# Optimization experiments

Hardware: AMD Instinct MI355X
Metric: run time of the kernel (lower is better)

## Reference

```python
import jax, jax.numpy as jnp
import numpy as np

H = 16          # num_heads
WIN = 512       # window_size


def setup_inputs() -> dict:
    key = jax.random.key(0)
    ks = jax.random.split(key, 4)
    B, S, D = 1, 4096, 1024
    s = 1.0 / np.sqrt(D)
    x = jax.random.normal(ks[0], (B, S, D), jnp.float32)
    Wqkv = jax.random.normal(ks[1], (3 * D, D), jnp.float32) * s
    bqkv = jnp.zeros((3 * D,), jnp.float32)
    Wout = jax.random.normal(ks[2], (D, D), jnp.float32) * s
    bout = jnp.zeros((D,), jnp.float32)
    return {"x": x, "Wqkv": Wqkv, "bqkv": bqkv, "Wout": Wout, "bout": bout}


def reference(x, Wqkv, bqkv, Wout, bout):
    B, S, D = x.shape
    d = D // H
    pads = WIN // 2
    C = WIN                 # chunk of query tokens processed together
    N = S // C              # number of chunks
    L = C + WIN - 1         # key-block length covering all windows in a chunk

    qkv = (x @ Wqkv.T + bqkv).reshape(B, S, 3, H, d).transpose(2, 0, 3, 1, 4)
    q, k, v = qkv[0], qkv[1], qkv[2]          # [B,H,S,d]

    # zero-pad K/V exactly like F.pad(..., value=0.0) in the original
    kp = jnp.pad(k, ((0, 0), (0, 0), (pads, pads), (0, 0)))
    vp = jnp.pad(v, ((0, 0), (0, 0), (pads, pads), (0, 0)))

    # gather overlapping key/value blocks: chunk n covers padded idx [n*C, n*C+L)
    idx = jnp.arange(N)[:, None] * C + jnp.arange(L)[None, :]   # [N,L]
    kb = kp[:, :, idx, :]                      # [B,H,N,L,d]
    vb = vp[:, :, idx, :]
    qc = q.reshape(B, H, N, C, d)

    scores = jnp.einsum('bhncd,bhnld->bhncl', qc, kb) / np.sqrt(d).astype(np.float32)
    c = jnp.arange(C)[:, None]
    j = jnp.arange(L)[None, :]
    band = (j >= c) & (j < c + WIN)            # [C,L]; zero-pad keys stay IN (score 0), matching original
    scores = jnp.where(band, scores, -jnp.inf)
    attn = jax.nn.softmax(scores, axis=-1)

    o = jnp.einsum('bhncl,bhnld->bhncd', attn, vb).reshape(B, H, S, d)
    o = o.transpose(0, 2, 1, 3).reshape(B, S, D)
    return o @ Wout.T + bout
```

## Files before the change

kernel.cpp:

```cpp
#include <hip/hip_runtime.h>


typedef __bf16 bf16x8 __attribute__((ext_vector_type(8)));
typedef float f32x4 __attribute__((ext_vector_type(4)));
typedef unsigned short u16;
typedef unsigned int u32;

#define MFMA16(a, b, c) __builtin_amdgcn_mfma_f32_16x16x32_bf16(a, b, c, 0, 0, 0)

__device__ __forceinline__ u16 f2b(float f) {
  union { float f; u32 u; } x; x.f = f;
  u32 r = x.u + 0x7fffu + ((x.u >> 16) & 1u);
  return (u16)(r >> 16);
}

union U8x16 { int4 v; u16 u[8]; };

__device__ __forceinline__ void gll16(const u16* g, u16* l) {
  __builtin_amdgcn_global_load_lds(
      (const __attribute__((address_space(1))) u16*)g,
      (__attribute__((address_space(3))) u16*)l, 16, 0, 0);
}

__global__ void cvt_all(const float* __restrict__ x, const float* __restrict__ wqkv,
                        const float* __restrict__ wout, u16* __restrict__ dst,
                        u16* __restrict__ Kp, u16* __restrict__ VTp)
{
  const int i = blockIdx.x * blockDim.x + threadIdx.x;
  if (i < 1048576) {
    const float* src; int off;
    if (i < 524288)       { src = x;    off = i; }
    else if (i < 917504)  { src = wqkv; off = i - 524288; }
    else                  { src = wout; off = i - 917504; }
    const float4 a = ((const float4*)src)[off * 2];
    const float4 b = ((const float4*)src)[off * 2 + 1];
    U8x16 t;
    t.u[0] = f2b(a.x); t.u[1] = f2b(a.y); t.u[2] = f2b(a.z); t.u[3] = f2b(a.w);
    t.u[4] = f2b(b.x); t.u[5] = f2b(b.y); t.u[6] = f2b(b.z); t.u[7] = f2b(b.w);
    ((int4*)dst)[i] = t.v;
    return;
  }
  const int j = i - 1048576;
  const int4 z = {0, 0, 0, 0};
  if (j < 65536) {
    const int h = j >> 12, rem = j & 4095;
    const int row512 = rem >> 3, c8 = (rem & 7) * 8;
    const int row = (row512 < 256) ? row512 : (4096 + row512);
    *(int4*)(&Kp[((long)h * 4608 + row) * 64 + c8]) = z;
  } else {
    const int j2 = j - 65536;
    const int h = j2 >> 12, rem = j2 & 4095;
    const int d = rem >> 6, kc = rem & 63;
    const int key = (kc < 32) ? kc * 8 : (4096 + kc * 8);
    *(int4*)(&VTp[((long)h * 64 + d) * 4608 + key]) = z;
  }
}

__global__ __launch_bounds__(256, 6) void gemm_qkv(
    const u16* __restrict__ A, const u16* __restrict__ B,
    const float* __restrict__ bias,
    u16* __restrict__ Qb, u16* __restrict__ Kp, u16* __restrict__ VTp)
{
  __shared__ u16 smem[12288];
  u16* const As = smem;
  u16* const Bs = smem + 4096;

  const int K = 1024;
  const int tid  = threadIdx.x;
  const int lane = tid & 63;
  const int wave = tid >> 6;
  const int quad = lane >> 4;
  const int c16  = lane & 15;
  const int wr   = wave >> 1;
  const int wc   = wave & 1;
  const long m0 = (long)blockIdx.y * 64;
  const long n0 = (long)blockIdx.x * 128;

  const int rowo   = lane >> 3;
  const int schunk = (lane & 7) ^ rowo;
  const u16* gA0 = &A[(m0 + wave * 16 + rowo) * K + schunk * 8];
  const u16* gA1 = gA0 + 8 * K;
  const u16* gB0 = &B[(n0 + wave * 32 + rowo) * K + schunk * 8];
  const u16* gB1 = gB0 + 8 * K;
  const u16* gB2 = gB0 + 16 * K;
  const u16* gB3 = gB0 + 24 * K;
  u16* const lA0 = &As[(wave * 16) * 64];
  u16* const lA1 = lA0 + 8 * 64;
  u16* const lB0 = &Bs[(wave * 32) * 64];
  u16* const lB1 = lB0 + 8 * 64;
  u16* const lB2 = lB0 + 16 * 64;
  u16* const lB3 = lB0 + 24 * 64;

  const int rsw  = c16 & 7;
  const int off0 = (quad ^ rsw) * 8;
  const int off1 = ((4 + quad) ^ rsw) * 8;
  const u16* rA[2]; const u16* rB[4];
#pragma unroll
  for (int i = 0; i < 2; ++i) rA[i] = &As[(wr * 32 + i * 16 + c16) * 64];
#pragma unroll
  for (int j = 0; j < 4; ++j) rB[j] = &Bs[(wc * 64 + j * 16 + c16) * 64];

  f32x4 acc[2][4];
#pragma unroll
  for (int i = 0; i < 2; ++i)
#pragma unroll
    for (int j = 0; j < 4; ++j)
      acc[i][j] = f32x4{0.f, 0.f, 0.f, 0.f};

  for (int k0 = 0; k0 < K; k0 += 64) {
    __syncthreads();
    gll16(gA0, lA0); gll16(gA1, lA1);
    gll16(gB0, lB0); gll16(gB1, lB1); gll16(gB2, lB2); gll16(gB3, lB3);
    gA0 += 64; gA1 += 64; gB0 += 64; gB1 += 64; gB2 += 64; gB3 += 64;
    __syncthreads();

#pragma unroll
    for (int h = 0; h < 2; ++h) {
      const int off = h ? off1 : off0;
      bf16x8 af[2], bfr[4];
#pragma unroll
      for (int i = 0; i < 2; ++i) af[i]  = *(const bf16x8*)(rA[i] + off);
#pragma unroll
      for (int j = 0; j < 4; ++j) bfr[j] = *(const bf16x8*)(rB[j] + off);
#pragma unroll
      for (int i = 0; i < 2; ++i)
#pragma unroll
        for (int j = 0; j < 4; ++j)
          acc[i][j] = MFMA16(af[i], bfr[j], acc[i][j]);
    }
  }

  const int region = (int)(n0 >> 10);
  if (region == 2) {
    __syncthreads();
    u16* const Ts = smem;
#pragma unroll
    for (int i = 0; i < 2; ++i)
#pragma unroll
      for (int j = 0; j < 4; ++j) {
        const int col = wc * 64 + j * 16 + c16;
        const float bv = bias[n0 + col];
#pragma unroll
        for (int r = 0; r < 4; ++r) {
          const int key  = wr * 32 + i * 16 + quad * 4 + r;
          const int slot = (key >> 3) ^ (col & 7);
          Ts[col * 64 + slot * 8 + (key & 7)] = f2b(acc[i][j][r] + bv);
        }
      }
    __syncthreads();
    const int base_n1 = (int)(n0 - 2048);
#pragma unroll
    for (int k = 0; k < 4; ++k) {
      const int idx  = k * 256 + tid;
      const int col  = idx >> 3, kc = idx & 7;
      const int slot = kc ^ (col & 7);
      const int4 v = *(const int4*)(&Ts[col * 64 + slot * 8]);
      const int n1 = base_n1 + col;
      const int h = n1 >> 6, d = n1 & 63;
      *(int4*)(&VTp[((long)h * 64 + d) * 4608 + 256 + m0 + kc * 8]) = v;
    }
    return;
  }

#pragma unroll
  for (int i = 0; i < 2; ++i) {
    const long row0 = m0 + wr * 32 + i * 16 + quad * 4;
#pragma unroll
    for (int j = 0; j < 4; ++j) {
      const long col = n0 + wc * 64 + j * 16 + c16;
      const float bv = bias[col];
      if (region == 0) {
#pragma unroll
        for (int r = 0; r < 4; ++r)
          Qb[(row0 + r) * 1024 + col] = f2b(acc[i][j][r] + bv);
      } else {
        const int n1 = (int)(col - 1024);
        const int h = n1 >> 6, d = n1 & 63;
#pragma unroll
        for (int r = 0; r < 4; ++r)
          Kp[((long)h * 4608 + row0 + r + 256) * 64 + d] = f2b(acc[i][j][r] + bv);
      }
    }
  }
}

__global__ __launch_bounds__(256, 4) void gemm_out(
    const u16* __restrict__ A, const u16* __restrict__ B,
    const float* __restrict__ bias, float* __restrict__ C)
{
  __shared__ u16 As[64 * 64];
  __shared__ u16 Bs[64 * 64];

  const int K = 1024, N = 1024;
  const int tid  = threadIdx.x;
  const int lane = tid & 63;
  const int wave = tid >> 6;
  const int quad = lane >> 4;
  const int c16  = lane & 15;
  const int wr   = wave >> 1;
  const int wc   = wave & 1;
  const long m0 = (long)blockIdx.y * 64;
  const long n0 = (long)blockIdx.x * 64;

  const int rowo   = lane >> 3;
  const int schunk = (lane & 7) ^ rowo;
  const u16* gA0 = &A[(m0 + wave * 16 + rowo) * K + schunk * 8];
  const u16* gA1 = gA0 + 8 * K;
  const u16* gB0 = &B[(n0 + wave * 16 + rowo) * K + schunk * 8];
  const u16* gB1 = gB0 + 8 * K;
  u16* const lA0 = &As[(wave * 16) * 64];
  u16* const lA1 = lA0 + 8 * 64;
  u16* const lB0 = &Bs[(wave * 16) * 64];
  u16* const lB1 = lB0 + 8 * 64;

  const int rsw  = c16 & 7;
  const int off0 = (quad ^ rsw) * 8;
  const int off1 = ((4 + quad) ^ rsw) * 8;
  const u16* rA[2]; const u16* rB[2];
#pragma unroll
  for (int i = 0; i < 2; ++i) {
    rA[i] = &As[(wr * 32 + i * 16 + c16) * 64];
    rB[i] = &Bs[(wc * 32 + i * 16 + c16) * 64];
  }

  f32x4 acc[2][2];
#pragma unroll
  for (int i = 0; i < 2; ++i)
#pragma unroll
    for (int j = 0; j < 2; ++j)
      acc[i][j] = f32x4{0.f, 0.f, 0.f, 0.f};

  for (int k0 = 0; k0 < K; k0 += 64) {
    __syncthreads();
    gll16(gA0, lA0); gll16(gA1, lA1);
    gll16(gB0, lB0); gll16(gB1, lB1);
    gA0 += 64; gA1 += 64; gB0 += 64; gB1 += 64;
    __syncthreads();

#pragma unroll
    for (int h = 0; h < 2; ++h) {
      const int off = h ? off1 : off0;
      bf16x8 af[2], bfr[2];
#pragma unroll
      for (int i = 0; i < 2; ++i) af[i]  = *(const bf16x8*)(rA[i] + off);
#pragma unroll
      for (int j = 0; j < 2; ++j) bfr[j] = *(const bf16x8*)(rB[j] + off);
#pragma unroll
      for (int i = 0; i < 2; ++i)
#pragma unroll
        for (int j = 0; j < 2; ++j)
          acc[i][j] = MFMA16(af[i], bfr[j], acc[i][j]);
    }
  }

#pragma unroll
  for (int i = 0; i < 2; ++i) {
    const long row0 = m0 + wr * 32 + i * 16 + quad * 4;
#pragma unroll
    for (int j = 0; j < 2; ++j) {
      const long col = n0 + wc * 32 + j * 16 + c16;
      const float bv = bias[col];
#pragma unroll
      for (int r = 0; r < 4; ++r)
        C[(row0 + r) * N + col] = acc[i][j][r] + bv;
    }
  }
}

__global__ __launch_bounds__(256, 4) void swa_fused(
    const u16* __restrict__ Qb, const u16* __restrict__ Kp,
    const u16* __restrict__ VTp, u16* __restrict__ o)
{
  __shared__ u16 Ks[64 * 64];
  __shared__ u16 Vs[64 * 64];
  __shared__ u16 Ps[4 * 16 * 64];

  const int tid  = threadIdx.x;
  const int lane = tid & 63;
  const int w    = tid >> 6;
  const int quad = lane >> 4;
  const int c16  = lane & 15;

  const int b    = blockIdx.x;
  const int xcd  = b & 7;
  const int idx  = b >> 3;
  const int h    = xcd * 2 + (idx >> 6);
  const int qb0  = (idx & 63) * 64;

  const long qrow = qb0 + w * 16 + c16;
  const bf16x8 aq0 = *(const bf16x8*)(&Qb[qrow * 1024 + h * 64 + quad * 8]);
  const bf16x8 aq1 = *(const bf16x8*)(&Qb[qrow * 1024 + h * 64 + 32 + quad * 8]);

  const int rowo   = lane >> 3;
  const int gchunk = (lane & 7) ^ rowo;
  const u16* gK0 = &Kp[((long)h * 4608 + qb0 + w * 16 + rowo) * 64 + gchunk * 8];
  const u16* gK1 = gK0 + 8 * 64;
  const u16* gV0 = &VTp[((long)h * 64 + w * 16 + rowo) * 4608 + qb0 + gchunk * 8];
  const u16* gV1 = gV0 + 8 * 4608;
  u16* const lK0 = &Ks[(w * 16) * 64];
  u16* const lK1 = lK0 + 8 * 64;
  u16* const lV0 = &Vs[(w * 16) * 64];
  u16* const lV1 = lV0 + 8 * 64;

  const int rsw  = c16 & 7;
  const int off0 = (quad ^ rsw) * 8;
  const int off1 = ((4 + quad) ^ rsw) * 8;
  const u16* rK[4]; const u16* rV[4];
#pragma unroll
  for (int i = 0; i < 4; ++i) {
    rK[i] = &Ks[(i * 16 + c16) * 64];
    rV[i] = &Vs[(i * 16 + c16) * 64];
  }
  u16* const Pw = &Ps[w * 1024];
  const u16* rP = &Pw[c16 * 64];

  const int dbase = c16 - 16 * w - quad * 4;

  f32x4 acc[4];
#pragma unroll
  for (int dt = 0; dt < 4; ++dt) acc[dt] = f32x4{0.f, 0.f, 0.f, 0.f};
  float rsum[4] = {0.f, 0.f, 0.f, 0.f};

  for (int t = 0; t < 9; ++t) {
    __syncthreads();
    gll16(gK0, lK0); gll16(gK1, lK1);
    gll16(gV0, lV0); gll16(gV1, lV1);
    gK0 += 64 * 64; gK1 += 64 * 64; gV0 += 64; gV1 += 64;
    __syncthreads();

#pragma unroll
    for (int tcol = 0; tcol < 4; ++tcol) {
      const bf16x8 bk0 = *(const bf16x8*)(rK[tcol] + off0);
      const bf16x8 bk1 = *(const bf16x8*)(rK[tcol] + off1);
      f32x4 s = f32x4{0.f, 0.f, 0.f, 0.f};
      s = MFMA16(aq0, bk0, s);
      s = MFMA16(aq1, bk1, s);
#pragma unroll
      for (int r = 0; r < 4; ++r) {
        const int delta = dbase + t * 64 + tcol * 16 - r;
        const float p = ((u32)delta < 512u) ? __expf(s[r] * 0.125f) : 0.f;
        rsum[r] += p;
        const int qi = quad * 4 + r;
        const int kc = tcol * 16 + c16;
        Pw[qi * 64 + (((kc >> 3) ^ (qi & 7)) * 8) + (kc & 7)] = f2b(p);
      }
    }

    const bf16x8 ap0 = *(const bf16x8*)(rP + off0);
    const bf16x8 ap1 = *(const bf16x8*)(rP + off1);
#pragma unroll
    for (int dt = 0; dt < 4; ++dt) {
      const bf16x8 bv0 = *(const bf16x8*)(rV[dt] + off0);
      const bf16x8 bv1 = *(const bf16x8*)(rV[dt] + off1);
      acc[dt] = MFMA16(ap0, bv0, acc[dt]);
      acc[dt] = MFMA16(ap1, bv1, acc[dt]);
    }
  }

#pragma unroll
  for (int off = 1; off < 16; off <<= 1)
#pragma unroll
    for (int r = 0; r < 4; ++r)
      rsum[r] += __shfl_xor(rsum[r], off, 64);

  const int qp = qb0 + w * 16 + quad * 4;
#pragma unroll
  for (int r = 0; r < 4; ++r) {
    const float inv = 1.f / rsum[r];
#pragma unroll
    for (int dt = 0; dt < 4; ++dt)
      o[(long)(qp + r) * 1024 + h * 64 + dt * 16 + c16] = f2b(acc[dt][r] * inv);
  }
}

extern "C" void kernel_launch(void* const* d_in, const int* in_sizes, int n_in,
                              void* d_out, int out_size, void* d_ws, size_t ws_size,
                              hipStream_t stream)
{
  const float* x    = (const float*)d_in[0];
  const float* Wqkv = (const float*)d_in[1];
  const float* bqkv = (const float*)d_in[2];
  const float* Wout = (const float*)d_in[3];
  const float* bout = (const float*)d_in[4];
  float* out = (float*)d_out;

  u16* xb    = (u16*)d_ws;
  u16* wqkvb = xb    + (size_t)4096 * 1024;
  u16* woutb = wqkvb + (size_t)3072 * 1024;
  u16* Qb    = woutb + (size_t)1024 * 1024;
  u16* Kp    = Qb    + (size_t)4096 * 1024;
  u16* VTp   = Kp    + (size_t)16 * 4608 * 64;
  u16* o     = VTp   + (size_t)16 * 4608 * 64;

  cvt_all<<<(1048576 + 131072) / 256, 256, 0, stream>>>(x, Wqkv, Wout, xb, Kp, VTp);

  gemm_qkv<<<dim3(3072 / 128, 4096 / 64), 256, 0, stream>>>(
      xb, wqkvb, bqkv, Qb, Kp, VTp);
  swa_fused<<<1024, 256, 0, stream>>>(Qb, Kp, VTp, o);
  gemm_out<<<dim3(1024 / 64, 4096 / 64), 256, 0, stream>>>(o, woutb, bout, out);
}
```

Measured before the change: 156.7 us.

## Load 128-key K/V tiles per sync and fold softmax scale into Q projection

The sliding-window attention kernel now stages 128 keys of K and V per iteration instead of 64, halving the number of barrier pairs (5 iterations instead of 9, last half-tile skipped). The LDS layout for V^T widens to 128 columns with a new 16-way XOR swizzle. The 1/sqrt(d) scale is moved into the QKV GEMM epilogue so the attention inner loop drops a multiply before exp. This doubles K/V shared memory per block, which may reduce occupancy, and the last iteration loads a half-tile that is never used.

```diff
diff --git a/kernel.cpp b/kernel.cpp
--- a/kernel.cpp
+++ b/kernel.cpp
@@ -172,7 +172,7 @@
       if (region == 0) {
 #pragma unroll
         for (int r = 0; r < 4; ++r)
-          Qb[(row0 + r) * 1024 + col] = f2b(acc[i][j][r] + bv);
+          Qb[(row0 + r) * 1024 + col] = f2b((acc[i][j][r] + bv) * 0.125f);
       } else {
         const int n1 = (int)(col - 1024);
         const int h = n1 >> 6, d = n1 & 63;
@@ -271,8 +271,8 @@
     const u16* __restrict__ Qb, const u16* __restrict__ Kp,
     const u16* __restrict__ VTp, u16* __restrict__ o)
 {
-  __shared__ u16 Ks[64 * 64];
-  __shared__ u16 Vs[64 * 64];
+  __shared__ u16 Ks[128 * 64];
+  __shared__ u16 Vs[64 * 128];
   __shared__ u16 Ps[4 * 16 * 64];
 
   const int tid  = threadIdx.x;
@@ -291,25 +291,34 @@
   const bf16x8 aq0 = *(const bf16x8*)(&Qb[qrow * 1024 + h * 64 + quad * 8]);
   const bf16x8 aq1 = *(const bf16x8*)(&Qb[qrow * 1024 + h * 64 + 32 + quad * 8]);
 
-  const int rowo   = lane >> 3;
-  const int gchunk = (lane & 7) ^ rowo;
-  const u16* gK0 = &Kp[((long)h * 4608 + qb0 + w * 16 + rowo) * 64 + gchunk * 8];
-  const u16* gK1 = gK0 + 8 * 64;
-  const u16* gV0 = &VTp[((long)h * 64 + w * 16 + rowo) * 4608 + qb0 + gchunk * 8];
-  const u16* gV1 = gV0 + 8 * 4608;
-  u16* const lK0 = &Ks[(w * 16) * 64];
-  u16* const lK1 = lK0 + 8 * 64;
-  u16* const lV0 = &Vs[(w * 16) * 64];
-  u16* const lV1 = lV0 + 8 * 64;
-
-  const int rsw  = c16 & 7;
-  const int off0 = (quad ^ rsw) * 8;
-  const int off1 = ((4 + quad) ^ rsw) * 8;
+  const int krow = lane >> 3;
+  const int kchk = (lane & 7) ^ krow;
+  const u16* gK = &Kp[((long)h * 4608 + qb0 + w * 32 + krow) * 64 + kchk * 8];
+  u16* const lK = &Ks[(w * 32) * 64];
+
+  const int vrow = lane >> 4;
+  const u16* gV[4]; u16* lV[4];
+#pragma unroll
+  for (int k = 0; k < 4; ++k) {
+    const int dlo  = 4 * k + vrow;
+    const int vchk = (lane & 15) ^ dlo;
+    gV[k] = &VTp[((long)h * 64 + w * 16 + dlo) * 4608 + qb0 + vchk * 8];
+    lV[k] = &Vs[(w * 16 + 4 * k) * 128];
+  }
+
+  const int off0 = (quad ^ (c16 & 7)) * 8;
+  const int off1 = ((4 + quad) ^ (c16 & 7)) * 8;
   const u16* rK[4]; const u16* rV[4];
 #pragma unroll
   for (int i = 0; i < 4; ++i) {
     rK[i] = &Ks[(i * 16 + c16) * 64];
-    rV[i] = &Vs[(i * 16 + c16) * 64];
+    rV[i] = &Vs[(i * 16 + c16) * 128];
+  }
+  int voff[2][2];
+#pragma unroll
+  for (int hf = 0; hf < 2; ++hf) {
+    voff[hf][0] = ((hf * 8 + quad) ^ c16) * 8;
+    voff[hf][1] = ((hf * 8 + 4 + quad) ^ c16) * 8;
   }
   u16* const Pw = &Ps[w * 1024];
   const u16* rP = &Pw[c16 * 64];
@@ -321,39 +330,49 @@
   for (int dt = 0; dt < 4; ++dt) acc[dt] = f32x4{0.f, 0.f, 0.f, 0.f};
   float rsum[4] = {0.f, 0.f, 0.f, 0.f};
 
-  for (int t = 0; t < 9; ++t) {
-    __syncthreads();
-    gll16(gK0, lK0); gll16(gK1, lK1);
-    gll16(gV0, lV0); gll16(gV1, lV1);
-    gK0 += 64 * 64; gK1 += 64 * 64; gV0 += 64; gV1 += 64;
-    __syncthreads();
-
-#pragma unroll
-    for (int tcol = 0; tcol < 4; ++tcol) {
-      const bf16x8 bk0 = *(const bf16x8*)(rK[tcol] + off0);
-      const bf16x8 bk1 = *(const bf16x8*)(rK[tcol] + off1);
-      f32x4 s = f32x4{0.f, 0.f, 0.f, 0.f};
-      s = MFMA16(aq0, bk0, s);
-      s = MFMA16(aq1, bk1, s);
-#pragma unroll
-      for (int r = 0; r < 4; ++r) {
-        const int delta = dbase + t * 64 + tcol * 16 - r;
-        const float p = ((u32)delta < 512u) ? __expf(s[r] * 0.125f) : 0.f;
-        rsum[r] += p;
-        const int qi = quad * 4 + r;
-        const int kc = tcol * 16 + c16;
-        Pw[qi * 64 + (((kc >> 3) ^ (qi & 7)) * 8) + (kc & 7)] = f2b(p);
+  for (int t = 0; t < 5; ++t) {
+    __syncthreads();
+    gll16(gK,            lK);
+    gll16(gK +  8 * 64,  lK +  8 * 64);
+    gll16(gK + 16 * 64,  lK + 16 * 64);
+    gll16(gK + 24 * 64,  lK + 24 * 64);
+#pragma unroll
+    for (int k = 0; k < 4; ++k) { gll16(gV[k], lV[k]); gV[k] += 128; }
+    gK += 128 * 64;
+    __syncthreads();
+
+#pragma unroll
+    for (int hf = 0; hf < 2; ++hf) {
+      if (t == 4 && hf == 1) break;
+
+#pragma unroll
+      for (int tcol = 0; tcol < 4; ++tcol) {
+        const u16* kb = rK[tcol] + hf * 64 * 64;
+        const bf16x8 bk0 = *(const bf16x8*)(kb + off0);
+        const bf16x8 bk1 = *(const bf16x8*)(kb + off1);
+        f32x4 s = f32x4{0.f, 0.f, 0.f, 0.f};
+        s = MFMA16(aq0, bk0, s);
+        s = MFMA16(aq1, bk1, s);
+#pragma unroll
+        for (int r = 0; r < 4; ++r) {
+          const int delta = dbase + t * 128 + hf * 64 + tcol * 16 - r;
+          const float p = ((u32)delta < 512u) ? __expf(s[r]) : 0.f;
+          rsum[r] += p;
+          const int qi = quad * 4 + r;
+          const int kc = tcol * 16 + c16;
+          Pw[qi * 64 + (((kc >> 3) ^ (qi & 7)) * 8) + (kc & 7)] = f2b(p);
+        }
       }
-    }
-
-    const bf16x8 ap0 = *(const bf16x8*)(rP + off0);
-    const bf16x8 ap1 = *(const bf16x8*)(rP + off1);
-#pragma unroll
-    for (int dt = 0; dt < 4; ++dt) {
-      const bf16x8 bv0 = *(const bf16x8*)(rV[dt] + off0);
-      const bf16x8 bv1 = *(const bf16x8*)(rV[dt] + off1);
-      acc[dt] = MFMA16(ap0, bv0, acc[dt]);
-      acc[dt] = MFMA16(ap1, bv1, acc[dt]);
+
+      const bf16x8 ap0 = *(const bf16x8*)(rP + off0);
+      const bf16x8 ap1 = *(const bf16x8*)(rP + off1);
+#pragma unroll
+      for (int dt = 0; dt < 4; ++dt) {
+        const bf16x8 bv0 = *(const bf16x8*)(rV[dt] + voff[hf][0]);
+        const bf16x8 bv1 = *(const bf16x8*)(rV[dt] + voff[hf][1]);
+        acc[dt] = MFMA16(ap0, bv0, acc[dt]);
+        acc[dt] = MFMA16(ap1, bv1, acc[dt]);
+      }
     }
   }
 
```

New measurement: 157.7 us (median of 2 runs). About the same (+0.6%).
